# Kernel optimization log

Hardware: AMD Instinct MI355X
Metric: run time of the kernel (lower is better)

The kernel has to match this reference:

```python
import jax, jax.numpy as jnp
import numpy as np

B, S, E = 8, 1025, 768
H, D = 12, 64  # num_heads, head_dim


def setup_inputs() -> dict:
    key = jax.random.key(0)
    ks = jax.random.split(key, 11)
    sc = 1.0 / np.sqrt(E)
    def lin(k):
        kw, kb = jax.random.split(k)
        return (jax.random.normal(kw, (E, E), jnp.float32) * sc,
                jax.random.normal(kb, (E,), jnp.float32) * sc)
    Wq, bq = lin(ks[0]); Wk, bk = lin(ks[1]); Wv, bv = lin(ks[2])
    Wc, bc = lin(ks[3]); Wo, bo = lin(ks[4])
    x = jax.random.normal(ks[5], (B, S, E), jnp.float32)
    return {"x": x, "Wq": Wq, "bq": bq, "Wk": Wk, "bk": bk,
            "Wv": Wv, "bv": bv, "Wc": Wc, "bc": bc, "Wo": Wo, "bo": bo}


def _heads(y, b, n):
    # [b, n, E] -> [b, H, n, D]
    return y.reshape(b, n, H, D).transpose(0, 2, 1, 3)


def reference(x, Wq, bq, Wk, bk, Wv, bv, Wc, bc, Wo, bo):
    b, s, e = x.shape
    n = s - 1  # special_cls strips the CLS token
    cls_token = x[:, 0, :]            # [b, E]
    xt = x[:, 1:, :]                  # [b, n, E]

    q = _heads(xt @ Wq.T + bq, b, n)  # [b, H, n, D]
    k = _heads(xt @ Wk.T + bk, b, n)
    v = _heads(xt @ Wv.T + bv, b, n)

    qk_dot = jnp.einsum('bhqd,bhkd->bhqk', q, k)             # [b,H,n,n]
    q_norm2 = jnp.clip((q ** 2).sum(-1, keepdims=True), 1e-5)  # [b,H,n,1]

    c = (cls_token @ Wc.T + bc).reshape(b, 1, H, D).transpose(0, 2, 1, 3)  # [b,H,1,D]
    cq_dot = jnp.einsum('bhod,bhqd->bhoq', c, q)             # [b,H,1,n]
    c_norm2 = jnp.clip((c ** 2).sum(-1, keepdims=True), 1e-5)  # [b,H,1,1]

    attn_logits = qk_dot * cq_dot.transpose(0, 1, 3, 2) / (q_norm2 * jnp.sqrt(D * c_norm2))

    ck_dot = jnp.einsum('bhod,bhkd->bhok', c, k)             # [b,H,1,n]
    attn_logits_for_cls = ck_dot / jnp.sqrt(D * c_norm2)
    cls_out = jnp.einsum('bhok,bhkd->bhod', attn_logits_for_cls, v).reshape(b, 1, H * D)

    attn = jax.nn.softmax(attn_logits, axis=-1)              # [b,H,n,n]
    values = jnp.einsum('bhqk,bhkd->bhqd', attn, v)          # [b,H,n,D]

    cls_out = (cls_token[:, None, :] + cls_out) * 0.5        # [b,1,E]
    values = jnp.concatenate(
        [cls_out, values.transpose(0, 2, 1, 3).reshape(b, n, e)], axis=1)  # [b,S,E]
    out = values @ Wo.T + bo
    return out, attn
```

## Files before the change

### kernel.cpp

```cpp
#include <hip/hip_runtime.h>

#define B_ 8
#define S_ 1025
#define E_ 768
#define H_ 12
#define D_ 64
#define N_ 1024
#define M_OUT (B_*S_)

typedef _Float16 half8_t __attribute__((ext_vector_type(8)));
typedef short short8_t __attribute__((ext_vector_type(8)));
typedef float f32x4 __attribute__((ext_vector_type(4)));

#define MFMA_F16(A, B, C)  __builtin_amdgcn_mfma_f32_16x16x32_f16((A), (B), (C), 0, 0, 0)
#define MFMA_BF16(A, B, C) __builtin_amdgcn_mfma_f32_16x16x32_bf16((A), (B), (C), 0, 0, 0)

__device__ __forceinline__ unsigned short f2bf(float f) {
  unsigned u = __float_as_uint(f);
  u += 0x7FFFu + ((u >> 16) & 1u);
  return (unsigned short)(u >> 16);
}
__device__ __forceinline__ float bf2f(unsigned short s) {
  return __uint_as_float(((unsigned)s) << 16);
}

__global__ __launch_bounds__(256) void proj_qkv_kernel(
    const float* __restrict__ x,
    const float* __restrict__ Wq, const float* __restrict__ bq,
    const float* __restrict__ Wk, const float* __restrict__ bk,
    const float* __restrict__ Wv, const float* __restrict__ bv,
    float* __restrict__ qo, float* __restrict__ ko, float* __restrict__ vo)
{
  __shared__ _Float16 Ah[128][40];
  __shared__ _Float16 Al[128][40];
  __shared__ _Float16 Bh[128][40];
  __shared__ _Float16 Bl[128][40];

  const int which = blockIdx.z;
  const float* __restrict__ W    = (which == 0) ? Wq : (which == 1) ? Wk : Wv;
  const float* __restrict__ bias = (which == 0) ? bq : (which == 1) ? bk : bv;
  float* __restrict__ out        = (which == 0) ? qo : (which == 1) ? ko : vo;

  const int tid  = threadIdx.x;
  const int lane = tid & 63;
  const int wv   = tid >> 6;
  const int wm   = wv >> 1, wn = wv & 1;
  const int m0   = blockIdx.y * 128;
  const int n0   = blockIdx.x * 128;

  const int srow = tid >> 1;
  const int scol = (tid & 1) << 4;

  const int gm = m0 + srow;
  const float* __restrict__ aptr = x + (long)(gm + (gm >> 10) + 1) * E_ + scol;
  const float* __restrict__ bptr = W + (long)(n0 + srow) * E_ + scol;

  f32x4 acc[4][4] = {};

  const int fr = lane & 15;
  const int kb = (lane >> 4) << 3;
  const int ar0 = wm * 64 + fr;
  const int br0 = wn * 64 + fr;

  for (int k0 = 0; k0 < E_; k0 += 32) {
    float4 a0 = *(const float4*)(aptr + k0);
    float4 a1 = *(const float4*)(aptr + k0 + 4);
    float4 a2 = *(const float4*)(aptr + k0 + 8);
    float4 a3 = *(const float4*)(aptr + k0 + 12);
    float4 b0 = *(const float4*)(bptr + k0);
    float4 b1 = *(const float4*)(bptr + k0 + 4);
    float4 b2 = *(const float4*)(bptr + k0 + 8);
    float4 b3 = *(const float4*)(bptr + k0 + 12);
    __syncthreads();
    {
      float av[16] = {a0.x,a0.y,a0.z,a0.w,a1.x,a1.y,a1.z,a1.w,
                      a2.x,a2.y,a2.z,a2.w,a3.x,a3.y,a3.z,a3.w};
      float bvv[16] = {b0.x,b0.y,b0.z,b0.w,b1.x,b1.y,b1.z,b1.w,
                       b2.x,b2.y,b2.z,b2.w,b3.x,b3.y,b3.z,b3.w};
      half8_t ah0, ah1, alo0, alo1, bh0, bh1, blo0, blo1;
      #pragma unroll
      for (int t = 0; t < 8; ++t) {
        _Float16 hh;
        hh = (_Float16)av[t];      ah0[t]  = hh; alo0[t] = (_Float16)(av[t]   - (float)hh);
        hh = (_Float16)av[t+8];    ah1[t]  = hh; alo1[t] = (_Float16)(av[t+8] - (float)hh);
        hh = (_Float16)bvv[t];     bh0[t]  = hh; blo0[t] = (_Float16)(bvv[t]   - (float)hh);
        hh = (_Float16)bvv[t+8];   bh1[t]  = hh; blo1[t] = (_Float16)(bvv[t+8] - (float)hh);
      }
      *(half8_t*)&Ah[srow][scol]     = ah0;  *(half8_t*)&Ah[srow][scol + 8] = ah1;
      *(half8_t*)&Al[srow][scol]     = alo0; *(half8_t*)&Al[srow][scol + 8] = alo1;
      *(half8_t*)&Bh[srow][scol]     = bh0;  *(half8_t*)&Bh[srow][scol + 8] = bh1;
      *(half8_t*)&Bl[srow][scol]     = blo0; *(half8_t*)&Bl[srow][scol + 8] = blo1;
    }
    __syncthreads();

    half8_t fah[4], fal[4], fbh[4], fbl[4];
    #pragma unroll
    for (int mi = 0; mi < 4; ++mi) {
      fah[mi] = *(const half8_t*)&Ah[ar0 + mi*16][kb];
      fal[mi] = *(const half8_t*)&Al[ar0 + mi*16][kb];
    }
    #pragma unroll
    for (int ni = 0; ni < 4; ++ni) {
      fbh[ni] = *(const half8_t*)&Bh[br0 + ni*16][kb];
      fbl[ni] = *(const half8_t*)&Bl[br0 + ni*16][kb];
    }
    #pragma unroll
    for (int mi = 0; mi < 4; ++mi)
      #pragma unroll
      for (int ni = 0; ni < 4; ++ni) {
        acc[mi][ni] = MFMA_F16(fah[mi], fbh[ni], acc[mi][ni]);
        acc[mi][ni] = MFMA_F16(fal[mi], fbh[ni], acc[mi][ni]);
        acc[mi][ni] = MFMA_F16(fah[mi], fbl[ni], acc[mi][ni]);
      }
  }

  const int rr = (lane >> 4) << 2;
  #pragma unroll
  for (int ni = 0; ni < 4; ++ni) {
    const int c = n0 + wn*64 + ni*16 + fr;
    const float bb = bias[c];
    #pragma unroll
    for (int mi = 0; mi < 4; ++mi) {
      const long row = m0 + wm*64 + mi*16 + rr;
      float* op = out + row * E_ + c;
      op[0]          = acc[mi][ni][0] + bb;
      op[E_]         = acc[mi][ni][1] + bb;
      op[2*E_]       = acc[mi][ni][2] + bb;
      op[3*(long)E_] = acc[mi][ni][3] + bb;
    }
  }
}

__global__ __launch_bounds__(256) void proj_out_kernel(
    const float* __restrict__ A, const float* __restrict__ W,
    const float* __restrict__ bias, float* __restrict__ out)
{
  __shared__ _Float16 Ah[128][40];
  __shared__ _Float16 Al[128][40];
  __shared__ _Float16 Bh[128][40];
  __shared__ _Float16 Bl[128][40];

  const int tid  = threadIdx.x;
  const int lane = tid & 63;
  const int wv   = tid >> 6;
  const int wm   = wv >> 1, wn = wv & 1;
  const int m0   = blockIdx.y * 128;
  const int n0   = blockIdx.x * 128;

  const int srow = tid >> 1;
  const int scol = (tid & 1) << 4;

  const int gm = m0 + srow;
  const bool aok = gm < M_OUT;
  const float* __restrict__ aptr = A + (long)gm * E_ + scol;
  const float* __restrict__ bptr = W + (long)(n0 + srow) * E_ + scol;

  f32x4 acc[4][4] = {};

  const int fr = lane & 15;
  const int kb = (lane >> 4) << 3;
  const int ar0 = wm * 64 + fr;
  const int br0 = wn * 64 + fr;

  for (int k0 = 0; k0 < E_; k0 += 32) {
    float4 a0 = make_float4(0.f,0.f,0.f,0.f), a1 = a0, a2 = a0, a3 = a0;
    if (aok) {
      a0 = *(const float4*)(aptr + k0);
      a1 = *(const float4*)(aptr + k0 + 4);
      a2 = *(const float4*)(aptr + k0 + 8);
      a3 = *(const float4*)(aptr + k0 + 12);
    }
    float4 b0 = *(const float4*)(bptr + k0);
    float4 b1 = *(const float4*)(bptr + k0 + 4);
    float4 b2 = *(const float4*)(bptr + k0 + 8);
    float4 b3 = *(const float4*)(bptr + k0 + 12);
    __syncthreads();
    {
      float av[16] = {a0.x,a0.y,a0.z,a0.w,a1.x,a1.y,a1.z,a1.w,
                      a2.x,a2.y,a2.z,a2.w,a3.x,a3.y,a3.z,a3.w};
      float bvv[16] = {b0.x,b0.y,b0.z,b0.w,b1.x,b1.y,b1.z,b1.w,
                       b2.x,b2.y,b2.z,b2.w,b3.x,b3.y,b3.z,b3.w};
      half8_t ah0, ah1, alo0, alo1, bh0, bh1, blo0, blo1;
      #pragma unroll
      for (int t = 0; t < 8; ++t) {
        _Float16 hh;
        hh = (_Float16)av[t];      ah0[t]  = hh; alo0[t] = (_Float16)(av[t]   - (float)hh);
        hh = (_Float16)av[t+8];    ah1[t]  = hh; alo1[t] = (_Float16)(av[t+8] - (float)hh);
        hh = (_Float16)bvv[t];     bh0[t]  = hh; blo0[t] = (_Float16)(bvv[t]   - (float)hh);
        hh = (_Float16)bvv[t+8];   bh1[t]  = hh; blo1[t] = (_Float16)(bvv[t+8] - (float)hh);
      }
      *(half8_t*)&Ah[srow][scol]     = ah0;  *(half8_t*)&Ah[srow][scol + 8] = ah1;
      *(half8_t*)&Al[srow][scol]     = alo0; *(half8_t*)&Al[srow][scol + 8] = alo1;
      *(half8_t*)&Bh[srow][scol]     = bh0;  *(half8_t*)&Bh[srow][scol + 8] = bh1;
      *(half8_t*)&Bl[srow][scol]     = blo0; *(half8_t*)&Bl[srow][scol + 8] = blo1;
    }
    __syncthreads();

    half8_t fah[4], fal[4], fbh[4], fbl[4];
    #pragma unroll
    for (int mi = 0; mi < 4; ++mi) {
      fah[mi] = *(const half8_t*)&Ah[ar0 + mi*16][kb];
      fal[mi] = *(const half8_t*)&Al[ar0 + mi*16][kb];
    }
    #pragma unroll
    for (int ni = 0; ni < 4; ++ni) {
      fbh[ni] = *(const half8_t*)&Bh[br0 + ni*16][kb];
      fbl[ni] = *(const half8_t*)&Bl[br0 + ni*16][kb];
    }
    #pragma unroll
    for (int mi = 0; mi < 4; ++mi)
      #pragma unroll
      for (int ni = 0; ni < 4; ++ni) {
        acc[mi][ni] = MFMA_F16(fah[mi], fbh[ni], acc[mi][ni]);
        acc[mi][ni] = MFMA_F16(fal[mi], fbh[ni], acc[mi][ni]);
        acc[mi][ni] = MFMA_F16(fah[mi], fbl[ni], acc[mi][ni]);
      }
  }

  const int rr = (lane >> 4) << 2;
  #pragma unroll
  for (int ni = 0; ni < 4; ++ni) {
    const int c = n0 + wn*64 + ni*16 + fr;
    const float bb = bias[c];
    #pragma unroll
    for (int mi = 0; mi < 4; ++mi) {
      const int row = m0 + wm*64 + mi*16 + rr;
      #pragma unroll
      for (int j = 0; j < 4; ++j) {
        if (row + j < M_OUT)
          out[(long)(row + j) * E_ + c] = acc[mi][ni][j] + bb;
      }
    }
  }
}

__global__ __launch_bounds__(64) void cls_c_kernel(
    const float* __restrict__ x, const float* __restrict__ Wc, const float* __restrict__ bc,
    float* __restrict__ cbuf, float* __restrict__ cdenom)
{
  const int bh = blockIdx.x;
  const int b = bh / H_, h = bh % H_;
  const int d = threadIdx.x;
  const float* xr = x + (long)b*S_*E_;
  const float* wr = Wc + (long)(h*D_ + d)*E_;
  float acc = 0.f;
  for (int j = 0; j < E_; j += 4) {
    float4 xw = *(const float4*)&xr[j];
    float4 ww = *(const float4*)&wr[j];
    acc += xw.x*ww.x + xw.y*ww.y + xw.z*ww.z + xw.w*ww.w;
  }
  acc += bc[h*D_ + d];
  cbuf[bh*D_ + d] = acc;
  float sq = acc*acc;
  #pragma unroll
  for (int off = 32; off > 0; off >>= 1) sq += __shfl_xor(sq, off);
  if (d == 0) cdenom[bh] = rsqrtf((float)D_ * fmaxf(sq, 1e-5f));
}

__global__ __launch_bounds__(256) void attn_kernel(
    const float* __restrict__ qbuf, const float* __restrict__ kbuf, const float* __restrict__ vbuf,
    const float* __restrict__ cbuf, const float* __restrict__ cdenom,
    float* __restrict__ vals, float* __restrict__ rowl_g, float* __restrict__ attn)
{
  __shared__ short QPh[64][72];
  __shared__ short QPl[64][72];
  __shared__ short Kh[64][72];
  __shared__ short Kl[64][72];
  __shared__ short Vth[64][72];
  __shared__ short Vtl[64][72];
  __shared__ float cs[64];
  __shared__ float rowscale_s[64];
  __shared__ float rowsum2[2][64];

  const int qt = blockIdx.x, h = blockIdx.y, b = blockIdx.z;
  const int bh = b * H_ + h;
  const int q0 = qt * 64;
  const int tid  = threadIdx.x;
  const int lane = tid & 63;
  const int wv   = tid >> 6;
  const int wm   = wv >> 1, wn = wv & 1;
  const int fr   = lane & 15;
  const int g    = lane >> 4;
  const int lr   = tid >> 2;
  const int lc   = (tid & 3) * 16;

  {
    const float* src = &qbuf[((long)b*N_ + q0 + lr)*E_ + h*D_ + lc];
    float4 t0 = *(const float4*)(src);
    float4 t1 = *(const float4*)(src+4);
    float4 t2 = *(const float4*)(src+8);
    float4 t3 = *(const float4*)(src+12);
    float tmp[16] = {t0.x,t0.y,t0.z,t0.w,t1.x,t1.y,t1.z,t1.w,
                     t2.x,t2.y,t2.z,t2.w,t3.x,t3.y,t3.z,t3.w};
    half8_t h0, h1, l0, l1;
    #pragma unroll
    for (int t = 0; t < 8; ++t) {
      _Float16 hh;
      hh = (_Float16)tmp[t];   h0[t] = hh; l0[t] = (_Float16)(tmp[t]   - (float)hh);
      hh = (_Float16)tmp[t+8]; h1[t] = hh; l1[t] = (_Float16)(tmp[t+8] - (float)hh);
    }
    *(half8_t*)&QPh[lr][lc]   = h0; *(half8_t*)&QPh[lr][lc+8] = h1;
    *(half8_t*)&QPl[lr][lc]   = l0; *(half8_t*)&QPl[lr][lc+8] = l1;
  }
  if (tid < 64) cs[tid] = cbuf[bh*D_ + tid];
  const float cdn = cdenom[bh];
  __syncthreads();

  if (tid < 64) {
    const _Float16* qh = (const _Float16*)QPh[tid];
    const _Float16* ql = (const _Float16*)QPl[tid];
    float qn2 = 0.f, cq = 0.f;
    #pragma unroll 8
    for (int d = 0; d < 64; ++d) {
      float qv = (float)qh[d] + (float)ql[d];
      qn2 = fmaf(qv, qv, qn2);
      cq  = fmaf(cs[d], qv, cq);
    }
    rowscale_s[tid] = cq * cdn / fmaxf(qn2, 1e-5f);
  }

  half8_t qfh[2][2], qfl[2][2];
  #pragma unroll
  for (int mi = 0; mi < 2; ++mi)
    #pragma unroll
    for (int ks = 0; ks < 2; ++ks) {
      qfh[mi][ks] = *(const half8_t*)&QPh[wm*32 + mi*16 + fr][ks*32 + g*8];
      qfl[mi][ks] = *(const half8_t*)&QPl[wm*32 + mi*16 + fr][ks*32 + g*8];
    }
  __syncthreads();

  float rs[2][4];
  #pragma unroll
  for (int mi = 0; mi < 2; ++mi)
    #pragma unroll
    for (int j = 0; j < 4; ++j)
      rs[mi][j] = rowscale_s[wm*32 + mi*16 + g*4 + j];

  float psum[2][4] = {};
  f32x4 acc[2][2] = {};

  for (int kt = 0; kt < 16; ++kt) {
    __syncthreads();
    {
      const float* src = &kbuf[((long)b*N_ + kt*64 + lr)*E_ + h*D_ + lc];
      float4 t0 = *(const float4*)(src);
      float4 t1 = *(const float4*)(src+4);
      float4 t2 = *(const float4*)(src+8);
      float4 t3 = *(const float4*)(src+12);
      float tmp[16] = {t0.x,t0.y,t0.z,t0.w,t1.x,t1.y,t1.z,t1.w,
                       t2.x,t2.y,t2.z,t2.w,t3.x,t3.y,t3.z,t3.w};
      half8_t h0, h1, l0, l1;
      #pragma unroll
      for (int t = 0; t < 8; ++t) {
        _Float16 hh;
        hh = (_Float16)tmp[t];   h0[t] = hh; l0[t] = (_Float16)(tmp[t]   - (float)hh);
        hh = (_Float16)tmp[t+8]; h1[t] = hh; l1[t] = (_Float16)(tmp[t+8] - (float)hh);
      }
      *(half8_t*)&Kh[lr][lc]   = h0; *(half8_t*)&Kh[lr][lc+8] = h1;
      *(half8_t*)&Kl[lr][lc]   = l0; *(half8_t*)&Kl[lr][lc+8] = l1;
    }
    {
      const float* src = &vbuf[((long)b*N_ + kt*64 + lr)*E_ + h*D_ + lc];
      float4 t0 = *(const float4*)(src);
      float4 t1 = *(const float4*)(src+4);
      float4 t2 = *(const float4*)(src+8);
      float4 t3 = *(const float4*)(src+12);
      float tmp[16] = {t0.x,t0.y,t0.z,t0.w,t1.x,t1.y,t1.z,t1.w,
                       t2.x,t2.y,t2.z,t2.w,t3.x,t3.y,t3.z,t3.w};
      #pragma unroll
      for (int t = 0; t < 16; ++t) {
        float f = tmp[t];
        unsigned short hb = f2bf(f);
        Vth[lc+t][lr] = (short)hb;
        Vtl[lc+t][lr] = (short)f2bf(f - bf2f(hb));
      }
    }
    __syncthreads();

    f32x4 sacc[2][2] = {};
    #pragma unroll
    for (int ks = 0; ks < 2; ++ks) {
      half8_t kfh[2], kfl[2];
      #pragma unroll
      for (int ni = 0; ni < 2; ++ni) {
        kfh[ni] = *(const half8_t*)&Kh[wn*32 + ni*16 + fr][ks*32 + g*8];
        kfl[ni] = *(const half8_t*)&Kl[wn*32 + ni*16 + fr][ks*32 + g*8];
      }
      #pragma unroll
      for (int mi = 0; mi < 2; ++mi)
        #pragma unroll
        for (int ni = 0; ni < 2; ++ni) {
          sacc[mi][ni] = MFMA_F16(qfh[mi][ks], kfh[ni], sacc[mi][ni]);
          sacc[mi][ni] = MFMA_F16(qfl[mi][ks], kfh[ni], sacc[mi][ni]);
          sacc[mi][ni] = MFMA_F16(qfh[mi][ks], kfl[ni], sacc[mi][ni]);
        }
    }

    #pragma unroll
    for (int mi = 0; mi < 2; ++mi)
      #pragma unroll
      for (int ni = 0; ni < 2; ++ni)
        #pragma unroll
        for (int j = 0; j < 4; ++j) {
          const int row = wm*32 + mi*16 + g*4 + j;
          const int col = wn*32 + ni*16 + fr;
          float s = sacc[mi][ni][j] * rs[mi][j];
          float p = __expf(fminf(s, 60.f));
          psum[mi][j] += p;
          attn[((long)(bh*N_ + q0 + row) << 10) + kt*64 + col] = p;
          unsigned short hb = f2bf(p);
          QPh[row][col] = (short)hb;
          QPl[row][col] = (short)f2bf(p - bf2f(hb));
        }
    __syncthreads();

    #pragma unroll
    for (int ks = 0; ks < 2; ++ks) {
      short8_t pfh[2], pfl[2], vfh[2], vfl[2];
      #pragma unroll
      for (int mi = 0; mi < 2; ++mi) {
        pfh[mi] = *(const short8_t*)&QPh[wm*32 + mi*16 + fr][ks*32 + g*8];
        pfl[mi] = *(const short8_t*)&QPl[wm*32 + mi*16 + fr][ks*32 + g*8];
      }
      #pragma unroll
      for (int nj = 0; nj < 2; ++nj) {
        vfh[nj] = *(const short8_t*)&Vth[wn*32 + nj*16 + fr][ks*32 + g*8];
        vfl[nj] = *(const short8_t*)&Vtl[wn*32 + nj*16 + fr][ks*32 + g*8];
      }
      #pragma unroll
      for (int mi = 0; mi < 2; ++mi)
        #pragma unroll
        for (int nj = 0; nj < 2; ++nj) {
          acc[mi][nj] = MFMA_BF16(pfh[mi], vfh[nj], acc[mi][nj]);
          acc[mi][nj] = MFMA_BF16(pfl[mi], vfh[nj], acc[mi][nj]);
          acc[mi][nj] = MFMA_BF16(pfh[mi], vfl[nj], acc[mi][nj]);
        }
    }
  }

  #pragma unroll
  for (int mi = 0; mi < 2; ++mi)
    #pragma unroll
    for (int j = 0; j < 4; ++j) {
      float v = psum[mi][j];
      v += __shfl_xor(v, 1);
      v += __shfl_xor(v, 2);
      v += __shfl_xor(v, 4);
      v += __shfl_xor(v, 8);
      psum[mi][j] = v;
    }
  __syncthreads();
  if (fr == 0) {
    #pragma unroll
    for (int mi = 0; mi < 2; ++mi)
      #pragma unroll
      for (int j = 0; j < 4; ++j)
        rowsum2[wn][wm*32 + mi*16 + g*4 + j] = psum[mi][j];
  }
  __syncthreads();

  if (tid < 64)
    rowl_g[(long)bh*N_ + q0 + tid] = rowsum2[0][tid] + rowsum2[1][tid];

  #pragma unroll
  for (int mi = 0; mi < 2; ++mi)
    #pragma unroll
    for (int j = 0; j < 4; ++j) {
      const int row = wm*32 + mi*16 + g*4 + j;
      const float inv = 1.0f / (rowsum2[0][row] + rowsum2[1][row]);
      #pragma unroll
      for (int nj = 0; nj < 2; ++nj) {
        const int col = wn*32 + nj*16 + fr;
        vals[((long)b*S_ + 1 + q0 + row)*E_ + h*D_ + col] = acc[mi][nj][j] * inv;
      }
    }
}

__global__ __launch_bounds__(256) void cls_attn_kernel(
    const float* __restrict__ x, const float* __restrict__ kbuf, const float* __restrict__ vbuf,
    const float* __restrict__ cbuf, const float* __restrict__ cdenom, float* __restrict__ vals)
{
  __shared__ float cs[64];
  __shared__ float part[4][64];
  const int bh = blockIdx.x;
  const int b = bh / H_, h = bh % H_;
  const int tid = threadIdx.x;
  const int wv = tid >> 6, lane = tid & 63;
  if (tid < 64) cs[tid] = cbuf[bh*D_ + tid];
  __syncthreads();
  float acc = 0.f;
  const long base0 = (long)b*N_*E_ + h*D_ + lane;
  for (int kk = wv*256; kk < wv*256 + 256; ++kk) {
    const long base = base0 + (long)kk*E_;
    float s = cs[lane] * kbuf[base];
    s += __shfl_xor(s, 1);  s += __shfl_xor(s, 2);  s += __shfl_xor(s, 4);
    s += __shfl_xor(s, 8);  s += __shfl_xor(s, 16); s += __shfl_xor(s, 32);
    acc = fmaf(s, vbuf[base], acc);
  }
  part[wv][lane] = acc;
  __syncthreads();
  if (tid < 64) {
    const float tot = (part[0][tid] + part[1][tid] + part[2][tid] + part[3][tid]) * cdenom[bh];
    const float cls = x[(long)b*S_*E_ + h*D_ + tid];
    vals[(long)b*S_*E_ + h*D_ + tid] = (cls + tot) * 0.5f;
  }
}

__global__ __launch_bounds__(256) void rescale_kernel(
    float* __restrict__ attn, const float* __restrict__ rowl_g)
{
  const long row = blockIdx.x;
  const float inv = 1.0f / rowl_g[row];
  float* p = attn + (row << 10) + threadIdx.x * 4;
  float4 u = *(float4*)p;
  u.x *= inv; u.y *= inv; u.z *= inv; u.w *= inv;
  *(float4*)p = u;
}

extern "C" void kernel_launch(void* const* d_in, const int* in_sizes, int n_in,
                              void* d_out, int out_size, void* d_ws, size_t ws_size,
                              hipStream_t stream) {
  (void)in_sizes; (void)n_in; (void)out_size; (void)ws_size;
  const float* x  = (const float*)d_in[0];
  const float* Wq = (const float*)d_in[1];
  const float* bq = (const float*)d_in[2];
  const float* Wk = (const float*)d_in[3];
  const float* bk = (const float*)d_in[4];
  const float* Wv = (const float*)d_in[5];
  const float* bv = (const float*)d_in[6];
  const float* Wc = (const float*)d_in[7];
  const float* bc = (const float*)d_in[8];
  const float* Wo = (const float*)d_in[9];
  const float* bo = (const float*)d_in[10];

  float* outp = (float*)d_out;
  float* attn = outp + (long)B_*S_*E_;

  float* qb   = (float*)d_ws;
  float* kb   = qb + (long)B_*N_*E_;
  float* vb   = kb + (long)B_*N_*E_;
  float* vals = vb + (long)B_*N_*E_;
  float* cbuf = vals + (long)B_*S_*E_;
  float* cden = cbuf + B_*H_*D_;
  float* rowl = cden + B_*H_;

  proj_qkv_kernel<<<dim3(6, 64, 3), 256, 0, stream>>>(x, Wq, bq, Wk, bk, Wv, bv, qb, kb, vb);
  cls_c_kernel<<<B_*H_, 64, 0, stream>>>(x, Wc, bc, cbuf, cden);
  attn_kernel<<<dim3(16, H_, B_), 256, 0, stream>>>(qb, kb, vb, cbuf, cden, vals, rowl, attn);
  cls_attn_kernel<<<B_*H_, 256, 0, stream>>>(x, kb, vb, cbuf, cden, vals);
  rescale_kernel<<<B_*H_*N_, 256, 0, stream>>>(attn, rowl);
  proj_out_kernel<<<dim3(6, 65), 256, 0, stream>>>(vals, Wo, bo, outp);
}
```

Baseline: 1.023 ms.

## Pre-split inputs and intermediates into fp16/bf16 hi-lo pairs once

Adds kernels that split x and the weights into high and low half-precision parts once, instead of redoing that split inside every GEMM tile. The projection kernels now write Q/K as fp16 hi/lo and V as a pre-transposed bf16 hi/lo layout, so the attention kernel loads ready-made fragments without conversion or a strided transpose. The attention output is also written as a split pair for the output projection. This cuts repeated conversion work and the scattered V transpose stores, at the cost of extra split passes, scattered transposed writes in the V epilogue, and using the attn output region as scratch before it is written.

```diff
diff --git a/kernel.cpp b/kernel.cpp
--- a/kernel.cpp
+++ b/kernel.cpp
@@ -9,6 +9,7 @@
 #define M_OUT (B_*S_)
 
 typedef _Float16 half8_t __attribute__((ext_vector_type(8)));
+typedef _Float16 half4_t __attribute__((ext_vector_type(4)));
 typedef short short8_t __attribute__((ext_vector_type(8)));
 typedef float f32x4 __attribute__((ext_vector_type(4)));
 
@@ -24,12 +25,60 @@
   return __uint_as_float(((unsigned)s) << 16);
 }
 
+__global__ __launch_bounds__(256) void split_x_kernel(
+    const float* __restrict__ x, _Float16* __restrict__ xh, _Float16* __restrict__ xl)
+{
+  const int idx = blockIdx.x * 256 + threadIdx.x;
+  const int row = idx / 192;
+  const int c   = (idx % 192) * 4;
+  const int xrow = row + (row >> 10) + 1;
+  float4 v = *(const float4*)&x[(long)xrow*E_ + c];
+  float f[4] = {v.x, v.y, v.z, v.w};
+  half4_t hs, ls;
+  #pragma unroll
+  for (int t = 0; t < 4; ++t) {
+    _Float16 hh = (_Float16)f[t];
+    hs[t] = hh; ls[t] = (_Float16)(f[t] - (float)hh);
+  }
+  *(half4_t*)&xh[(long)row*E_ + c] = hs;
+  *(half4_t*)&xl[(long)row*E_ + c] = ls;
+}
+
+__global__ __launch_bounds__(256) void split_w_kernel(
+    const float* __restrict__ W0, const float* __restrict__ W1,
+    const float* __restrict__ W2, const float* __restrict__ W3,
+    _Float16* __restrict__ h0, _Float16* __restrict__ l0,
+    _Float16* __restrict__ h1, _Float16* __restrict__ l1,
+    _Float16* __restrict__ h2, _Float16* __restrict__ l2,
+    _Float16* __restrict__ h3, _Float16* __restrict__ l3)
+{
+  const int which = blockIdx.y;
+  const float* __restrict__ W = (which==0)?W0:(which==1)?W1:(which==2)?W2:W3;
+  _Float16* __restrict__ oh   = (which==0)?h0:(which==1)?h1:(which==2)?h2:h3;
+  _Float16* __restrict__ ol   = (which==0)?l0:(which==1)?l1:(which==2)?l2:l3;
+  const int idx = blockIdx.x * 256 + threadIdx.x;
+  const long off = (long)idx * 4;
+  float4 v = *(const float4*)&W[off];
+  float f[4] = {v.x, v.y, v.z, v.w};
+  half4_t hs, ls;
+  #pragma unroll
+  for (int t = 0; t < 4; ++t) {
+    _Float16 hh = (_Float16)f[t];
+    hs[t] = hh; ls[t] = (_Float16)(f[t] - (float)hh);
+  }
+  *(half4_t*)&oh[off] = hs;
+  *(half4_t*)&ol[off] = ls;
+}
+
 __global__ __launch_bounds__(256) void proj_qkv_kernel(
-    const float* __restrict__ x,
-    const float* __restrict__ Wq, const float* __restrict__ bq,
-    const float* __restrict__ Wk, const float* __restrict__ bk,
-    const float* __restrict__ Wv, const float* __restrict__ bv,
-    float* __restrict__ qo, float* __restrict__ ko, float* __restrict__ vo)
+    const _Float16* __restrict__ xh, const _Float16* __restrict__ xl,
+    const _Float16* __restrict__ wqh, const _Float16* __restrict__ wql,
+    const _Float16* __restrict__ wkh, const _Float16* __restrict__ wkl,
+    const _Float16* __restrict__ wvh, const _Float16* __restrict__ wvl,
+    const float* __restrict__ bq, const float* __restrict__ bk, const float* __restrict__ bv,
+    _Float16* __restrict__ qh, _Float16* __restrict__ ql,
+    _Float16* __restrict__ kh, _Float16* __restrict__ kl,
+    unsigned short* __restrict__ vth, unsigned short* __restrict__ vtl)
 {
   __shared__ _Float16 Ah[128][40];
   __shared__ _Float16 Al[128][40];
@@ -37,9 +86,9 @@
   __shared__ _Float16 Bl[128][40];
 
   const int which = blockIdx.z;
-  const float* __restrict__ W    = (which == 0) ? Wq : (which == 1) ? Wk : Wv;
-  const float* __restrict__ bias = (which == 0) ? bq : (which == 1) ? bk : bv;
-  float* __restrict__ out        = (which == 0) ? qo : (which == 1) ? ko : vo;
+  const _Float16* __restrict__ wh = (which==0)?wqh:(which==1)?wkh:wvh;
+  const _Float16* __restrict__ wl = (which==0)?wql:(which==1)?wkl:wvl;
+  const float* __restrict__ bias  = (which==0)?bq:(which==1)?bk:bv;
 
   const int tid  = threadIdx.x;
   const int lane = tid & 63;
@@ -51,9 +100,8 @@
   const int srow = tid >> 1;
   const int scol = (tid & 1) << 4;
 
-  const int gm = m0 + srow;
-  const float* __restrict__ aptr = x + (long)(gm + (gm >> 10) + 1) * E_ + scol;
-  const float* __restrict__ bptr = W + (long)(n0 + srow) * E_ + scol;
+  const long arow = (long)(m0 + srow) * E_ + scol;
+  const long brow = (long)(n0 + srow) * E_ + scol;
 
   f32x4 acc[4][4] = {};
 
@@ -63,34 +111,19 @@
   const int br0 = wn * 64 + fr;
 
   for (int k0 = 0; k0 < E_; k0 += 32) {
-    float4 a0 = *(const float4*)(aptr + k0);
-    float4 a1 = *(const float4*)(aptr + k0 + 4);
-    float4 a2 = *(const float4*)(aptr + k0 + 8);
-    float4 a3 = *(const float4*)(aptr + k0 + 12);
-    float4 b0 = *(const float4*)(bptr + k0);
-    float4 b1 = *(const float4*)(bptr + k0 + 4);
-    float4 b2 = *(const float4*)(bptr + k0 + 8);
-    float4 b3 = *(const float4*)(bptr + k0 + 12);
+    half8_t a_h0 = *(const half8_t*)&xh[arow + k0];
+    half8_t a_h1 = *(const half8_t*)&xh[arow + k0 + 8];
+    half8_t a_l0 = *(const half8_t*)&xl[arow + k0];
+    half8_t a_l1 = *(const half8_t*)&xl[arow + k0 + 8];
+    half8_t b_h0 = *(const half8_t*)&wh[brow + k0];
+    half8_t b_h1 = *(const half8_t*)&wh[brow + k0 + 8];
+    half8_t b_l0 = *(const half8_t*)&wl[brow + k0];
+    half8_t b_l1 = *(const half8_t*)&wl[brow + k0 + 8];
     __syncthreads();
-    {
-      float av[16] = {a0.x,a0.y,a0.z,a0.w,a1.x,a1.y,a1.z,a1.w,
-                      a2.x,a2.y,a2.z,a2.w,a3.x,a3.y,a3.z,a3.w};
-      float bvv[16] = {b0.x,b0.y,b0.z,b0.w,b1.x,b1.y,b1.z,b1.w,
-                       b2.x,b2.y,b2.z,b2.w,b3.x,b3.y,b3.z,b3.w};
-      half8_t ah0, ah1, alo0, alo1, bh0, bh1, blo0, blo1;
-      #pragma unroll
-      for (int t = 0; t < 8; ++t) {
-        _Float16 hh;
-        hh = (_Float16)av[t];      ah0[t]  = hh; alo0[t] = (_Float16)(av[t]   - (float)hh);
-        hh = (_Float16)av[t+8];    ah1[t]  = hh; alo1[t] = (_Float16)(av[t+8] - (float)hh);
-        hh = (_Float16)bvv[t];     bh0[t]  = hh; blo0[t] = (_Float16)(bvv[t]   - (float)hh);
-        hh = (_Float16)bvv[t+8];   bh1[t]  = hh; blo1[t] = (_Float16)(bvv[t+8] - (float)hh);
-      }
-      *(half8_t*)&Ah[srow][scol]     = ah0;  *(half8_t*)&Ah[srow][scol + 8] = ah1;
-      *(half8_t*)&Al[srow][scol]     = alo0; *(half8_t*)&Al[srow][scol + 8] = alo1;
-      *(half8_t*)&Bh[srow][scol]     = bh0;  *(half8_t*)&Bh[srow][scol + 8] = bh1;
-      *(half8_t*)&Bl[srow][scol]     = blo0; *(half8_t*)&Bl[srow][scol + 8] = blo1;
-    }
+    *(half8_t*)&Ah[srow][scol]   = a_h0;  *(half8_t*)&Ah[srow][scol+8] = a_h1;
+    *(half8_t*)&Al[srow][scol]   = a_l0;  *(half8_t*)&Al[srow][scol+8] = a_l1;
+    *(half8_t*)&Bh[srow][scol]   = b_h0;  *(half8_t*)&Bh[srow][scol+8] = b_h1;
+    *(half8_t*)&Bl[srow][scol]   = b_l0;  *(half8_t*)&Bl[srow][scol+8] = b_l1;
     __syncthreads();
 
     half8_t fah[4], fal[4], fbh[4], fbl[4];
@@ -115,24 +148,52 @@
   }
 
   const int rr = (lane >> 4) << 2;
-  #pragma unroll
-  for (int ni = 0; ni < 4; ++ni) {
-    const int c = n0 + wn*64 + ni*16 + fr;
-    const float bb = bias[c];
-    #pragma unroll
-    for (int mi = 0; mi < 4; ++mi) {
-      const long row = m0 + wm*64 + mi*16 + rr;
-      float* op = out + row * E_ + c;
-      op[0]          = acc[mi][ni][0] + bb;
-      op[E_]         = acc[mi][ni][1] + bb;
-      op[2*E_]       = acc[mi][ni][2] + bb;
-      op[3*(long)E_] = acc[mi][ni][3] + bb;
+  if (which < 2) {
+    _Float16* __restrict__ oh = (which==0) ? qh : kh;
+    _Float16* __restrict__ ol = (which==0) ? ql : kl;
+    #pragma unroll
+    for (int ni = 0; ni < 4; ++ni) {
+      const int c = n0 + wn*64 + ni*16 + fr;
+      const float bb = bias[c];
+      #pragma unroll
+      for (int mi = 0; mi < 4; ++mi) {
+        const int row0 = m0 + wm*64 + mi*16 + rr;
+        #pragma unroll
+        for (int j = 0; j < 4; ++j) {
+          float r = acc[mi][ni][j] + bb;
+          _Float16 hh = (_Float16)r;
+          oh[(long)(row0+j)*E_ + c] = hh;
+          ol[(long)(row0+j)*E_ + c] = (_Float16)(r - (float)hh);
+        }
+      }
+    }
+  } else {
+    #pragma unroll
+    for (int ni = 0; ni < 4; ++ni) {
+      const int c = n0 + wn*64 + ni*16 + fr;
+      const int h_ = c >> 6, d_ = c & 63;
+      const float bb = bias[c];
+      #pragma unroll
+      for (int mi = 0; mi < 4; ++mi) {
+        const int row0 = m0 + wm*64 + mi*16 + rr;
+        #pragma unroll
+        for (int j = 0; j < 4; ++j) {
+          const int row = row0 + j;
+          const int b_ = row >> 10, n_ = row & 1023;
+          float r = acc[mi][ni][j] + bb;
+          unsigned short hb = f2bf(r);
+          const long o = ((long)(b_*H_ + h_)*64 + d_)*N_ + n_;
+          vth[o] = hb;
+          vtl[o] = f2bf(r - bf2f(hb));
+        }
+      }
     }
   }
 }
 
 __global__ __launch_bounds__(256) void proj_out_kernel(
-    const float* __restrict__ A, const float* __restrict__ W,
+    const _Float16* __restrict__ ah_g, const _Float16* __restrict__ al_g,
+    const _Float16* __restrict__ wh, const _Float16* __restrict__ wl,
     const float* __restrict__ bias, float* __restrict__ out)
 {
   __shared__ _Float16 Ah[128][40];
@@ -152,8 +213,8 @@
 
   const int gm = m0 + srow;
   const bool aok = gm < M_OUT;
-  const float* __restrict__ aptr = A + (long)gm * E_ + scol;
-  const float* __restrict__ bptr = W + (long)(n0 + srow) * E_ + scol;
+  const long arow = (long)gm * E_ + scol;
+  const long brow = (long)(n0 + srow) * E_ + scol;
 
   f32x4 acc[4][4] = {};
 
@@ -163,37 +224,22 @@
   const int br0 = wn * 64 + fr;
 
   for (int k0 = 0; k0 < E_; k0 += 32) {
-    float4 a0 = make_float4(0.f,0.f,0.f,0.f), a1 = a0, a2 = a0, a3 = a0;
+    half8_t a_h0 = {}, a_h1 = {}, a_l0 = {}, a_l1 = {};
     if (aok) {
-      a0 = *(const float4*)(aptr + k0);
-      a1 = *(const float4*)(aptr + k0 + 4);
-      a2 = *(const float4*)(aptr + k0 + 8);
-      a3 = *(const float4*)(aptr + k0 + 12);
-    }
-    float4 b0 = *(const float4*)(bptr + k0);
-    float4 b1 = *(const float4*)(bptr + k0 + 4);
-    float4 b2 = *(const float4*)(bptr + k0 + 8);
-    float4 b3 = *(const float4*)(bptr + k0 + 12);
+      a_h0 = *(const half8_t*)&ah_g[arow + k0];
+      a_h1 = *(const half8_t*)&ah_g[arow + k0 + 8];
+      a_l0 = *(const half8_t*)&al_g[arow + k0];
+      a_l1 = *(const half8_t*)&al_g[arow + k0 + 8];
+    }
+    half8_t b_h0 = *(const half8_t*)&wh[brow + k0];
+    half8_t b_h1 = *(const half8_t*)&wh[brow + k0 + 8];
+    half8_t b_l0 = *(const half8_t*)&wl[brow + k0];
+    half8_t b_l1 = *(const half8_t*)&wl[brow + k0 + 8];
     __syncthreads();
-    {
-      float av[16] = {a0.x,a0.y,a0.z,a0.w,a1.x,a1.y,a1.z,a1.w,
-                      a2.x,a2.y,a2.z,a2.w,a3.x,a3.y,a3.z,a3.w};
-      float bvv[16] = {b0.x,b0.y,b0.z,b0.w,b1.x,b1.y,b1.z,b1.w,
-                       b2.x,b2.y,b2.z,b2.w,b3.x,b3.y,b3.z,b3.w};
-      half8_t ah0, ah1, alo0, alo1, bh0, bh1, blo0, blo1;
-      #pragma unroll
-      for (int t = 0; t < 8; ++t) {
-        _Float16 hh;
-        hh = (_Float16)av[t];      ah0[t]  = hh; alo0[t] = (_Float16)(av[t]   - (float)hh);
-        hh = (_Float16)av[t+8];    ah1[t]  = hh; alo1[t] = (_Float16)(av[t+8] - (float)hh);
-        hh = (_Float16)bvv[t];     bh0[t]  = hh; blo0[t] = (_Float16)(bvv[t]   - (float)hh);
-        hh = (_Float16)bvv[t+8];   bh1[t]  = hh; blo1[t] = (_Float16)(bvv[t+8] - (float)hh);
-      }
-      *(half8_t*)&Ah[srow][scol]     = ah0;  *(half8_t*)&Ah[srow][scol + 8] = ah1;
-      *(half8_t*)&Al[srow][scol]     = alo0; *(half8_t*)&Al[srow][scol + 8] = alo1;
-      *(half8_t*)&Bh[srow][scol]     = bh0;  *(half8_t*)&Bh[srow][scol + 8] = bh1;
-      *(half8_t*)&Bl[srow][scol]     = blo0; *(half8_t*)&Bl[srow][scol + 8] = blo1;
-    }
+    *(half8_t*)&Ah[srow][scol]   = a_h0;  *(half8_t*)&Ah[srow][scol+8] = a_h1;
+    *(half8_t*)&Al[srow][scol]   = a_l0;  *(half8_t*)&Al[srow][scol+8] = a_l1;
+    *(half8_t*)&Bh[srow][scol]   = b_h0;  *(half8_t*)&Bh[srow][scol+8] = b_h1;
+    *(half8_t*)&Bl[srow][scol]   = b_l0;  *(half8_t*)&Bl[srow][scol+8] = b_l1;
     __syncthreads();
 
     half8_t fah[4], fal[4], fbh[4], fbl[4];
@@ -258,16 +304,19 @@
 }
 
 __global__ __launch_bounds__(256) void attn_kernel(
-    const float* __restrict__ qbuf, const float* __restrict__ kbuf, const float* __restrict__ vbuf,
+    const _Float16* __restrict__ qh, const _Float16* __restrict__ ql,
+    const _Float16* __restrict__ kh, const _Float16* __restrict__ kl,
+    const unsigned short* __restrict__ vth, const unsigned short* __restrict__ vtl,
     const float* __restrict__ cbuf, const float* __restrict__ cdenom,
-    float* __restrict__ vals, float* __restrict__ rowl_g, float* __restrict__ attn)
+    _Float16* __restrict__ valsh, _Float16* __restrict__ vall,
+    float* __restrict__ rowl_g, float* __restrict__ attn)
 {
   __shared__ short QPh[64][72];
   __shared__ short QPl[64][72];
-  __shared__ short Kh[64][72];
-  __shared__ short Kl[64][72];
-  __shared__ short Vth[64][72];
-  __shared__ short Vtl[64][72];
+  __shared__ short Kh_s[64][72];
+  __shared__ short Kl_s[64][72];
+  __shared__ short Vth_s[64][72];
+  __shared__ short Vtl_s[64][72];
   __shared__ float cs[64];
   __shared__ float rowscale_s[64];
   __shared__ float rowsum2[2][64];
@@ -285,34 +334,23 @@
   const int lc   = (tid & 3) * 16;
 
   {
-    const float* src = &qbuf[((long)b*N_ + q0 + lr)*E_ + h*D_ + lc];
-    float4 t0 = *(const float4*)(src);
-    float4 t1 = *(const float4*)(src+4);
-    float4 t2 = *(const float4*)(src+8);
-    float4 t3 = *(const float4*)(src+12);
-    float tmp[16] = {t0.x,t0.y,t0.z,t0.w,t1.x,t1.y,t1.z,t1.w,
-                     t2.x,t2.y,t2.z,t2.w,t3.x,t3.y,t3.z,t3.w};
-    half8_t h0, h1, l0, l1;
-    #pragma unroll
-    for (int t = 0; t < 8; ++t) {
-      _Float16 hh;
-      hh = (_Float16)tmp[t];   h0[t] = hh; l0[t] = (_Float16)(tmp[t]   - (float)hh);
-      hh = (_Float16)tmp[t+8]; h1[t] = hh; l1[t] = (_Float16)(tmp[t+8] - (float)hh);
-    }
-    *(half8_t*)&QPh[lr][lc]   = h0; *(half8_t*)&QPh[lr][lc+8] = h1;
-    *(half8_t*)&QPl[lr][lc]   = l0; *(half8_t*)&QPl[lr][lc+8] = l1;
+    const long qbase = ((long)b*N_ + q0 + lr)*E_ + h*D_ + lc;
+    *(half8_t*)&QPh[lr][lc]   = *(const half8_t*)&qh[qbase];
+    *(half8_t*)&QPh[lr][lc+8] = *(const half8_t*)&qh[qbase+8];
+    *(half8_t*)&QPl[lr][lc]   = *(const half8_t*)&ql[qbase];
+    *(half8_t*)&QPl[lr][lc+8] = *(const half8_t*)&ql[qbase+8];
   }
   if (tid < 64) cs[tid] = cbuf[bh*D_ + tid];
   const float cdn = cdenom[bh];
   __syncthreads();
 
   if (tid < 64) {
-    const _Float16* qh = (const _Float16*)QPh[tid];
-    const _Float16* ql = (const _Float16*)QPl[tid];
+    const _Float16* qhr = (const _Float16*)QPh[tid];
+    const _Float16* qlr = (const _Float16*)QPl[tid];
     float qn2 = 0.f, cq = 0.f;
     #pragma unroll 8
     for (int d = 0; d < 64; ++d) {
-      float qv = (float)qh[d] + (float)ql[d];
+      float qv = (float)qhr[d] + (float)qlr[d];
       qn2 = fmaf(qv, qv, qn2);
       cq  = fmaf(cs[d], qv, cq);
     }
@@ -342,38 +380,18 @@
   for (int kt = 0; kt < 16; ++kt) {
     __syncthreads();
     {
-      const float* src = &kbuf[((long)b*N_ + kt*64 + lr)*E_ + h*D_ + lc];
-      float4 t0 = *(const float4*)(src);
-      float4 t1 = *(const float4*)(src+4);
-      float4 t2 = *(const float4*)(src+8);
-      float4 t3 = *(const float4*)(src+12);
-      float tmp[16] = {t0.x,t0.y,t0.z,t0.w,t1.x,t1.y,t1.z,t1.w,
-                       t2.x,t2.y,t2.z,t2.w,t3.x,t3.y,t3.z,t3.w};
-      half8_t h0, h1, l0, l1;
-      #pragma unroll
-      for (int t = 0; t < 8; ++t) {
-        _Float16 hh;
-        hh = (_Float16)tmp[t];   h0[t] = hh; l0[t] = (_Float16)(tmp[t]   - (float)hh);
-        hh = (_Float16)tmp[t+8]; h1[t] = hh; l1[t] = (_Float16)(tmp[t+8] - (float)hh);
-      }
-      *(half8_t*)&Kh[lr][lc]   = h0; *(half8_t*)&Kh[lr][lc+8] = h1;
-      *(half8_t*)&Kl[lr][lc]   = l0; *(half8_t*)&Kl[lr][lc+8] = l1;
+      const long kbase = ((long)b*N_ + kt*64 + lr)*E_ + h*D_ + lc;
+      *(half8_t*)&Kh_s[lr][lc]   = *(const half8_t*)&kh[kbase];
+      *(half8_t*)&Kh_s[lr][lc+8] = *(const half8_t*)&kh[kbase+8];
+      *(half8_t*)&Kl_s[lr][lc]   = *(const half8_t*)&kl[kbase];
+      *(half8_t*)&Kl_s[lr][lc+8] = *(const half8_t*)&kl[kbase+8];
     }
     {
-      const float* src = &vbuf[((long)b*N_ + kt*64 + lr)*E_ + h*D_ + lc];
-      float4 t0 = *(const float4*)(src);
-      float4 t1 = *(const float4*)(src+4);
-      float4 t2 = *(const float4*)(src+8);
-      float4 t3 = *(const float4*)(src+12);
-      float tmp[16] = {t0.x,t0.y,t0.z,t0.w,t1.x,t1.y,t1.z,t1.w,
-                       t2.x,t2.y,t2.z,t2.w,t3.x,t3.y,t3.z,t3.w};
-      #pragma unroll
-      for (int t = 0; t < 16; ++t) {
-        float f = tmp[t];
-        unsigned short hb = f2bf(f);
-        Vth[lc+t][lr] = (short)hb;
-        Vtl[lc+t][lr] = (short)f2bf(f - bf2f(hb));
-      }
+      const long vbase = ((long)bh*64 + lr)*N_ + kt*64 + lc;
+      *(short8_t*)&Vth_s[lr][lc]   = *(const short8_t*)(vth + vbase);
+      *(short8_t*)&Vth_s[lr][lc+8] = *(const short8_t*)(vth + vbase + 8);
+      *(short8_t*)&Vtl_s[lr][lc]   = *(const short8_t*)(vtl + vbase);
+      *(short8_t*)&Vtl_s[lr][lc+8] = *(const short8_t*)(vtl + vbase + 8);
     }
     __syncthreads();
 
@@ -383,8 +401,8 @@
       half8_t kfh[2], kfl[2];
       #pragma unroll
       for (int ni = 0; ni < 2; ++ni) {
-        kfh[ni] = *(const half8_t*)&Kh[wn*32 + ni*16 + fr][ks*32 + g*8];
-        kfl[ni] = *(const half8_t*)&Kl[wn*32 + ni*16 + fr][ks*32 + g*8];
+        kfh[ni] = *(const half8_t*)&Kh_s[wn*32 + ni*16 + fr][ks*32 + g*8];
+        kfl[ni] = *(const half8_t*)&Kl_s[wn*32 + ni*16 + fr][ks*32 + g*8];
       }
       #pragma unroll
       for (int mi = 0; mi < 2; ++mi)
@@ -424,8 +442,8 @@
       }
       #pragma unroll
       for (int nj = 0; nj < 2; ++nj) {
-        vfh[nj] = *(const short8_t*)&Vth[wn*32 + nj*16 + fr][ks*32 + g*8];
-        vfl[nj] = *(const short8_t*)&Vtl[wn*32 + nj*16 + fr][ks*32 + g*8];
+        vfh[nj] = *(const short8_t*)&Vth_s[wn*32 + nj*16 + fr][ks*32 + g*8];
+        vfl[nj] = *(const short8_t*)&Vtl_s[wn*32 + nj*16 + fr][ks*32 + g*8];
       }
       #pragma unroll
       for (int mi = 0; mi < 2; ++mi)
@@ -471,14 +489,21 @@
       #pragma unroll
       for (int nj = 0; nj < 2; ++nj) {
         const int col = wn*32 + nj*16 + fr;
-        vals[((long)b*S_ + 1 + q0 + row)*E_ + h*D_ + col] = acc[mi][nj][j] * inv;
+        const long vo = ((long)b*S_ + 1 + q0 + row)*E_ + h*D_ + col;
+        float r = acc[mi][nj][j] * inv;
+        _Float16 hh = (_Float16)r;
+        valsh[vo] = hh;
+        vall[vo]  = (_Float16)(r - (float)hh);
       }
     }
 }
 
 __global__ __launch_bounds__(256) void cls_attn_kernel(
-    const float* __restrict__ x, const float* __restrict__ kbuf, const float* __restrict__ vbuf,
-    const float* __restrict__ cbuf, const float* __restrict__ cdenom, float* __restrict__ vals)
+    const float* __restrict__ x,
+    const _Float16* __restrict__ kh, const _Float16* __restrict__ kl,
+    const unsigned short* __restrict__ vth, const unsigned short* __restrict__ vtl,
+    const float* __restrict__ cbuf, const float* __restrict__ cdenom,
+    _Float16* __restrict__ valsh, _Float16* __restrict__ vall)
 {
   __shared__ float cs[64];
   __shared__ float part[4][64];
@@ -489,20 +514,27 @@
   if (tid < 64) cs[tid] = cbuf[bh*D_ + tid];
   __syncthreads();
   float acc = 0.f;
-  const long base0 = (long)b*N_*E_ + h*D_ + lane;
+  const long kbase0 = (long)b*N_*E_ + h*D_ + lane;
+  const long vtbase = ((long)bh*64 + lane)*N_;
   for (int kk = wv*256; kk < wv*256 + 256; ++kk) {
-    const long base = base0 + (long)kk*E_;
-    float s = cs[lane] * kbuf[base];
+    const long kbase = kbase0 + (long)kk*E_;
+    float kv = (float)kh[kbase] + (float)kl[kbase];
+    float s = cs[lane] * kv;
     s += __shfl_xor(s, 1);  s += __shfl_xor(s, 2);  s += __shfl_xor(s, 4);
     s += __shfl_xor(s, 8);  s += __shfl_xor(s, 16); s += __shfl_xor(s, 32);
-    acc = fmaf(s, vbuf[base], acc);
+    float vvv = bf2f(vth[vtbase + kk]) + bf2f(vtl[vtbase + kk]);
+    acc = fmaf(s, vvv, acc);
   }
   part[wv][lane] = acc;
   __syncthreads();
   if (tid < 64) {
     const float tot = (part[0][tid] + part[1][tid] + part[2][tid] + part[3][tid]) * cdenom[bh];
     const float cls = x[(long)b*S_*E_ + h*D_ + tid];
-    vals[(long)b*S_*E_ + h*D_ + tid] = (cls + tot) * 0.5f;
+    float r = (cls + tot) * 0.5f;
+    const long vo = (long)b*S_*E_ + h*D_ + tid;
+    _Float16 hh = (_Float16)r;
+    valsh[vo] = hh;
+    vall[vo]  = (_Float16)(r - (float)hh);
   }
 }
 
@@ -533,21 +565,46 @@
   const float* Wo = (const float*)d_in[9];
   const float* bo = (const float*)d_in[10];
 
+  const long XSZ = (long)8192 * E_;
+  const long WSZ = (long)E_ * E_;
+  const long QSZ = (long)B_ * N_ * E_;
+  const long VSZ = (long)B_ * S_ * E_;
+
   float* outp = (float*)d_out;
-  float* attn = outp + (long)B_*S_*E_;
-
-  float* qb   = (float*)d_ws;
-  float* kb   = qb + (long)B_*N_*E_;
-  float* vb   = kb + (long)B_*N_*E_;
-  float* vals = vb + (long)B_*N_*E_;
-  float* cbuf = vals + (long)B_*S_*E_;
+  float* attn = outp + VSZ;
+
+  _Float16* xh  = (_Float16*)attn;
+  _Float16* xl  = xh + XSZ;
+  _Float16* wqh = xl + XSZ;
+  _Float16* wql = wqh + WSZ;
+  _Float16* wkh = wql + WSZ;
+  _Float16* wkl = wkh + WSZ;
+  _Float16* wvh = wkl + WSZ;
+  _Float16* wvl = wvh + WSZ;
+
+  _Float16* qh = (_Float16*)d_ws;
+  _Float16* ql = qh + QSZ;
+  _Float16* kh = ql + QSZ;
+  _Float16* kl = kh + QSZ;
+  unsigned short* vth = (unsigned short*)(kl + QSZ);
+  unsigned short* vtl = vth + QSZ;
+  _Float16* valsh = (_Float16*)(vtl + QSZ);
+  _Float16* vall  = valsh + VSZ;
+  _Float16* woh   = vall + VSZ;
+  _Float16* wol   = woh + WSZ;
+  float* cbuf = (float*)(wol + WSZ);
   float* cden = cbuf + B_*H_*D_;
   float* rowl = cden + B_*H_;
 
-  proj_qkv_kernel<<<dim3(6, 64, 3), 256, 0, stream>>>(x, Wq, bq, Wk, bk, Wv, bv, qb, kb, vb);
+  split_x_kernel<<<6144, 256, 0, stream>>>(x, xh, xl);
+  split_w_kernel<<<dim3(576, 4), 256, 0, stream>>>(Wq, Wk, Wv, Wo,
+      wqh, wql, wkh, wkl, wvh, wvl, woh, wol);
+  proj_qkv_kernel<<<dim3(6, 64, 3), 256, 0, stream>>>(xh, xl,
+      wqh, wql, wkh, wkl, wvh, wvl, bq, bk, bv, qh, ql, kh, kl, vth, vtl);
   cls_c_kernel<<<B_*H_, 64, 0, stream>>>(x, Wc, bc, cbuf, cden);
-  attn_kernel<<<dim3(16, H_, B_), 256, 0, stream>>>(qb, kb, vb, cbuf, cden, vals, rowl, attn);
-  cls_attn_kernel<<<B_*H_, 256, 0, stream>>>(x, kb, vb, cbuf, cden, vals);
+  attn_kernel<<<dim3(16, H_, B_), 256, 0, stream>>>(qh, ql, kh, kl, vth, vtl,
+      cbuf, cden, valsh, vall, rowl, attn);
+  cls_attn_kernel<<<B_*H_, 256, 0, stream>>>(x, kh, kl, vth, vtl, cbuf, cden, valsh, vall);
   rescale_kernel<<<B_*H_*N_, 256, 0, stream>>>(attn, rowl);
-  proj_out_kernel<<<dim3(6, 65), 256, 0, stream>>>(vals, Wo, bo, outp);
-}
+  proj_out_kernel<<<dim3(6, 65), 256, 0, stream>>>(valsh, vall, woh, wol, bo, outp);
+}
```

After: 1.037 ms. Within noise of the previous version (+1.4%).
